# Performance work log

Measured on AMD Instinct MI355X. Metric: run time of the kernel, lower is better.

Reference implementation:

```python
import jax, jax.numpy as jnp
import numpy as np

N_ENT = 100000   # entities / graph nodes
N_REL = 500      # relations (table has 2*N_REL rows: fwd+inv)
H = 256          # hidden dim
E = 320000       # edges


def setup_inputs() -> dict:
    key = jax.random.key(0)
    ks = jax.random.split(key, 9)
    std = (2.0 / (H + H)) ** 0.5  # xavier_normal for (H,H)
    return {
        "ent_emb": jax.random.normal(ks[0], (N_ENT, H), dtype=jnp.float32),
        "rel_emb": jax.random.normal(ks[1], (2 * N_REL, H), dtype=jnp.float32),
        "w_edge": jax.random.normal(ks[2], (H, H), dtype=jnp.float32) * std,
        "w_node": jax.random.normal(ks[3], (H, H), dtype=jnp.float32) * std,
        "w_comp": jax.random.normal(ks[4], (H, H), dtype=jnp.float32) * std,
        "rel_w": jax.random.normal(ks[5], (H, H), dtype=jnp.float32) * std,
        "src": jax.random.randint(ks[6], (E,), 0, N_ENT, dtype=jnp.int32),
        "dst": jax.random.randint(ks[7], (E,), 0, N_ENT, dtype=jnp.int32),
        "rel_id": jax.random.randint(ks[8], (E,), 0, 2 * N_REL, dtype=jnp.int32),
        "node_id": jnp.arange(N_ENT, dtype=jnp.int32),
    }


def _edge_softmax(score, dst, n):
    # per-destination-node softmax over incoming edges (DGL edge_softmax)
    m = jax.ops.segment_max(score, dst, num_segments=n)
    ex = jnp.exp(score - m[dst])
    s = jax.ops.segment_sum(ex, dst, num_segments=n)
    return ex / s[dst]


def reference(ent_emb, rel_emb, w_edge, w_node, w_comp, rel_w,
              src, dst, rel_id, node_id):
    n = ent_emb.shape[0]
    h = ent_emb[node_id]          # [N, H] (node_id maps node -> entity row)
    hs = h[src]                   # [E, H] source node features
    hd = h[dst]                   # [E, H] destination node features
    e = rel_emb[rel_id]           # [E, H] edge (relation) features

    # EdgeLayer: e . h_dst -> edge_softmax -> scatter-sum(e * a) -> W -> tanh
    a_e = _edge_softmax(jnp.sum(e * hd, axis=-1), dst, n)
    edge_out = jnp.tanh(
        jax.ops.segment_sum(e * a_e[:, None], dst, num_segments=n) @ w_edge)

    # NodeLayer: h_src . h_dst -> edge_softmax -> scatter-sum(h_src * a)
    a_n = _edge_softmax(jnp.sum(hs * hd, axis=-1), dst, n)
    node_out = jnp.tanh(
        jax.ops.segment_sum(hs * a_n[:, None], dst, num_segments=n) @ w_node)

    # CompLayer (mul): comp = h_src * e ; comp . h_dst -> softmax -> scatter-sum
    comp = hs * e
    a_c = _edge_softmax(jnp.sum(comp * hd, axis=-1), dst, n)
    comp_out = jnp.tanh(
        jax.ops.segment_sum(comp * a_c[:, None], dst, num_segments=n) @ w_comp)

    out_ent = ent_emb + edge_out + node_out + comp_out
    out_rel = rel_emb @ rel_w
    return (out_ent, out_rel)
```

## Files before the change

### kernel.cpp

```cpp
#include <hip/hip_runtime.h>
#include <hip/hip_bf16.h>

#define N_ENT  100000
#define N_REL2 1000
#define H      256
#define E_EDGES 320000
#define REL_ROWS_PAD 1024
#define DEG_BINS 64

typedef unsigned short u16;
typedef short bf16x8 __attribute__((ext_vector_type(8)));
typedef float floatx4 __attribute__((ext_vector_type(4)));

__device__ __forceinline__ u16 f2bf(float f) {
    unsigned x = __float_as_uint(f);
    unsigned r = (x + 0x7fffu + ((x >> 16) & 1u)) >> 16;
    return (u16)r;
}

__device__ __forceinline__ ushort4 pack4(float4 v, float s) {
    return make_ushort4(f2bf(v.x * s), f2bf(v.y * s), f2bf(v.z * s), f2bf(v.w * s));
}

__device__ __forceinline__ float fast_tanh(float x) {
    float e = __expf(2.0f * x);
    return 1.0f - 2.0f * __builtin_amdgcn_rcpf(e + 1.0f);
}

__device__ __forceinline__ void async16(u16* lds, const u16* g) {
    __builtin_amdgcn_global_load_lds(
        (const __attribute__((address_space(1))) void*)g,
        (__attribute__((address_space(3))) void*)lds, 16, 0, 0);
}


__global__ void hist_kernel(const int* __restrict__ dst, int* __restrict__ counts) {
    int i = blockIdx.x * blockDim.x + threadIdx.x;
    if (i < E_EDGES) atomicAdd(&counts[dst[i]], 1);
}

__global__ void scan1_kernel(const int* __restrict__ counts, int* __restrict__ offsets,
                             int* __restrict__ bsum) {
    __shared__ int buf[1024];
    int t = threadIdx.x, i = blockIdx.x * 1024 + t;
    int v = (i < N_ENT) ? counts[i] : 0;
    int acc = v;
    buf[t] = acc;
    __syncthreads();
    for (int off = 1; off < 1024; off <<= 1) {
        int u = (t >= off) ? buf[t - off] : 0;
        __syncthreads();
        acc += u;
        buf[t] = acc;
        __syncthreads();
    }
    if (i < N_ENT) offsets[i] = acc - v;
    if (t == 1023) bsum[blockIdx.x] = acc;
}

__global__ void scan2_kernel(int* __restrict__ bsum, int* __restrict__ offsets) {
    __shared__ int s[128];
    int t = threadIdx.x;
    s[t] = (t < 98) ? bsum[t] : 0;
    __syncthreads();
    if (t == 0) {
        int run = 0;
        for (int b = 0; b < 98; ++b) { int x = s[b]; s[b] = run; run += x; }
        offsets[N_ENT] = run;
    }
    __syncthreads();
    if (t < 98) bsum[t] = s[t];
}

__global__ void scan3_kernel(int* __restrict__ offsets, const int* __restrict__ bsum) {
    int i = blockIdx.x * 1024 + threadIdx.x;
    if (i < N_ENT && blockIdx.x > 0) offsets[i] += bsum[blockIdx.x];
}


__global__ void deghist_kernel(const int* __restrict__ counts, int* __restrict__ dbin) {
    __shared__ int lh[DEG_BINS];
    int t = threadIdx.x;
    if (t < DEG_BINS) lh[t] = 0;
    __syncthreads();
    int i = blockIdx.x * blockDim.x + t;
    if (i < N_ENT) {
        int b = counts[i]; if (b > DEG_BINS - 1) b = DEG_BINS - 1;
        atomicAdd(&lh[b], 1);
    }
    __syncthreads();
    if (t < DEG_BINS && lh[t]) atomicAdd(&dbin[t], lh[t]);
}

__global__ void degscan_kernel(const int* __restrict__ dbin, int* __restrict__ doff) {
    if (threadIdx.x == 0) {
        int run = 0;
        for (int b = 0; b < DEG_BINS; ++b) { doff[b] = run; run += dbin[b]; }
    }
}

__global__ void degplace_kernel(const int* __restrict__ counts, int* __restrict__ doff,
                                int* __restrict__ dorder) {
    __shared__ int lh[DEG_BINS];
    __shared__ int lbase[DEG_BINS];
    int t = threadIdx.x;
    if (t < DEG_BINS) lh[t] = 0;
    __syncthreads();
    int i = blockIdx.x * blockDim.x + t;
    int b = 0, myidx = 0;
    if (i < N_ENT) {
        b = counts[i]; if (b > DEG_BINS - 1) b = DEG_BINS - 1;
        myidx = atomicAdd(&lh[b], 1);
    }
    __syncthreads();
    if (t < DEG_BINS) lbase[t] = lh[t] ? atomicAdd(&doff[t], lh[t]) : 0;
    __syncthreads();
    if (i < N_ENT) dorder[lbase[b] + myidx] = i;
}

__global__ void place_kernel(const int* __restrict__ dst, const int* __restrict__ src,
                             const int* __restrict__ rel_id, const int* __restrict__ node_id,
                             const int* __restrict__ offsets,
                             int* __restrict__ counts, int2* __restrict__ meta) {
    int i = blockIdx.x * blockDim.x + threadIdx.x;
    if (i < E_EDGES) {
        int d = dst[i];
        int old = atomicSub(&counts[d], 1);
        meta[offsets[d] + old - 1] = make_int2(node_id[src[i]], rel_id[i]);
    }
}

__global__ void swz_kernel(const float* __restrict__ w0, const float* __restrict__ w1,
                           const float* __restrict__ w2, const float* __restrict__ w3,
                           u16* __restrict__ dstp) {
    int t = blockIdx.x * blockDim.x + threadIdx.x;
    if (t >= 4 * H * H) return;
    int mat = t >> 16;
    int r = t & 65535;
    int j = r & 7, lane = (r >> 3) & 63, kstep = (r >> 9) & 7, ntile = r >> 12;
    int k = kstep * 32 + (lane >> 4) * 8 + j;
    int n = ntile * 16 + (lane & 15);
    const float* W = (mat == 0) ? w0 : (mat == 1) ? w1 : (mat == 2) ? w2 : w3;
    dstp[t] = f2bf(W[k * H + n]);
}

__global__ void relbf_kernel(const float* __restrict__ rel, u16* __restrict__ out) {
    int t = blockIdx.x * blockDim.x + threadIdx.x;
    if (t >= REL_ROWS_PAD * H) return;
    int row = t >> 8, kk = t & 255;
    int k = kk ^ ((row & 7) << 3);
    float v = (row < N_REL2) ? rel[row * H + k] : 0.f;
    out[t] = f2bf(v);
}

__global__ __launch_bounds__(256) void scatter_kernel(
    const float* __restrict__ ent, const float* __restrict__ rel,
    const int2* __restrict__ meta, const int* __restrict__ node_id,
    const int* __restrict__ offsets, const int* __restrict__ dorder,
    u16* __restrict__ agg_e, u16* __restrict__ agg_n, u16* __restrict__ agg_c) {
    int lane = threadIdx.x & 63;
    int wv = __builtin_amdgcn_readfirstlane(threadIdx.x >> 6);
    int w = blockIdx.x * 4 + wv;
    if (w >= N_ENT) return;
    int d = dorder[w];
    int nid = node_id[d];
    int p0 = offsets[d], p1 = offsets[d + 1];
    float4 hd = ((const float4*)(ent + (size_t)nid * H))[lane];
    float me = -INFINITY, mn = -INFINITY, mc = -INFINITY;
    float le = 0.f, ln = 0.f, lc = 0.f;
    float4 ae = make_float4(0, 0, 0, 0), an = make_float4(0, 0, 0, 0), ac = make_float4(0, 0, 0, 0);

    for (int pc = p0; pc < p1; pc += 4) {
        int cnt = p1 - pc; if (cnt > 4) cnt = 4;
        int2 md[4];
#pragma unroll
        for (int j = 0; j < 4; ++j) if (j < cnt) md[j] = meta[pc + j];
        float4 ev[4], sv[4];
#pragma unroll
        for (int j = 0; j < 4; ++j) if (j < cnt) {
            ev[j] = ((const float4*)(rel + (size_t)md[j].y * H))[lane];
            sv[j] = ((const float4*)(ent + (size_t)md[j].x * H))[lane];
        }
#pragma unroll
        for (int j = 0; j < 4; ++j) if (j < cnt) {
            float4 e4 = ev[j], s4 = sv[j];
            float4 c4 = make_float4(e4.x * s4.x, e4.y * s4.y, e4.z * s4.z, e4.w * s4.w);
            float de = e4.x * hd.x + e4.y * hd.y + e4.z * hd.z + e4.w * hd.w;
            float dn = s4.x * hd.x + s4.y * hd.y + s4.z * hd.z + s4.w * hd.w;
            float dc = c4.x * hd.x + c4.y * hd.y + c4.z * hd.z + c4.w * hd.w;
#pragma unroll
            for (int o = 32; o > 0; o >>= 1) {
                de += __shfl_xor(de, o);
                dn += __shfl_xor(dn, o);
                dc += __shfl_xor(dc, o);
            }
            { float nm = fmaxf(me, de); float s = __expf(me - nm); float pr = __expf(de - nm);
              le = le * s + pr;
              ae.x = ae.x * s + pr * e4.x; ae.y = ae.y * s + pr * e4.y;
              ae.z = ae.z * s + pr * e4.z; ae.w = ae.w * s + pr * e4.w; me = nm; }
            { float nm = fmaxf(mn, dn); float s = __expf(mn - nm); float pr = __expf(dn - nm);
              ln = ln * s + pr;
              an.x = an.x * s + pr * s4.x; an.y = an.y * s + pr * s4.y;
              an.z = an.z * s + pr * s4.z; an.w = an.w * s + pr * s4.w; mn = nm; }
            { float nm = fmaxf(mc, dc); float s = __expf(mc - nm); float pr = __expf(dc - nm);
              lc = lc * s + pr;
              ac.x = ac.x * s + pr * c4.x; ac.y = ac.y * s + pr * c4.y;
              ac.z = ac.z * s + pr * c4.z; ac.w = ac.w * s + pr * c4.w; mc = nm; }
        }
    }
    float ie = (le > 0.f) ? 1.0f / le : 0.f;
    float in_ = (ln > 0.f) ? 1.0f / ln : 0.f;
    float ic = (lc > 0.f) ? 1.0f / lc : 0.f;
    size_t rowb = (size_t)d * (H * 2);
    int boff = (lane * 8) ^ ((d & 7) << 4);
    *(ushort4*)((char*)agg_e + rowb + boff) = pack4(ae, ie);
    *(ushort4*)((char*)agg_n + rowb + boff) = pack4(an, in_);
    *(ushort4*)((char*)agg_c + rowb + boff) = pack4(ac, ic);
}

__global__ __launch_bounds__(256, 2) void gemm_kernel(
    const u16* __restrict__ A0, const u16* __restrict__ A1, const u16* __restrict__ A2,
    const u16* __restrict__ W0, const u16* __restrict__ W1, const u16* __restrict__ W2,
    const float* __restrict__ base, float* __restrict__ out,
    int n_real, int n_layers, int do_tanh) {
    __shared__ u16 lA[2][16384];
    int tid = threadIdx.x;
    int lane = tid & 63;
    int wv = tid >> 6;
    int m = lane & 15;
    int quad = lane >> 4;
    int r0 = blockIdx.x * 64;
    const u16* As[3] = { A0, A1, A2 };
    const u16* Ws[3] = { W0, W1, W2 };

    float outacc[4][4][4];
#pragma unroll
    for (int rt = 0; rt < 4; ++rt)
#pragma unroll
        for (int ct = 0; ct < 4; ++ct) {
            int grow = r0 + rt * 16 + quad * 4;
            int gcol = wv * 64 + ct * 16 + m;
#pragma unroll
            for (int r = 0; r < 4; ++r) {
                float v = 0.f;
                if (base != nullptr && (grow + r) < n_real) v = base[(size_t)(grow + r) * H + gcol];
                outacc[rt][ct][r] = v;
            }
        }

    {
        const u16* gsrc = As[0] + (size_t)blockIdx.x * 64 * H;
#pragma unroll
        for (int rnd = 0; rnd < 8; ++rnd) {
            int off8 = (rnd * 256 + tid) * 8;
            async16(&lA[0][off8], gsrc + off8);
        }
    }

    int mrow = m * 512;
    int swz = (m & 7) << 4;

    for (int l = 0; l < n_layers; ++l) {
        __syncthreads();
        if (l + 1 < n_layers) {
            const u16* gsrc = As[l + 1] + (size_t)blockIdx.x * 64 * H;
            u16* dstb = lA[(l + 1) & 1];
#pragma unroll
            for (int rnd = 0; rnd < 8; ++rnd) {
                int off8 = (rnd * 256 + tid) * 8;
                async16(&dstb[off8], gsrc + off8);
            }
        }
        const char* lbc = (const char*)lA[l & 1];
        const u16* Wl = Ws[l];

        floatx4 lacc[4][4];
#pragma unroll
        for (int rt = 0; rt < 4; ++rt)
#pragma unroll
            for (int ct = 0; ct < 4; ++ct)
#pragma unroll
                for (int r = 0; r < 4; ++r) lacc[rt][ct][r] = 0.f;

#pragma unroll
        for (int ks = 0; ks < 8; ++ks) {
            bf16x8 af[4], bfr[4];
#pragma unroll
            for (int rt = 0; rt < 4; ++rt)
                af[rt] = *(const bf16x8*)(lbc + rt * 8192 + mrow + ((ks * 64 + quad * 16) ^ swz));
#pragma unroll
            for (int ct = 0; ct < 4; ++ct)
                bfr[ct] = *(const bf16x8*)(Wl + (((size_t)(wv * 4 + ct) * 8 + ks) * 64 + lane) * 8);
#pragma unroll
            for (int rt = 0; rt < 4; ++rt)
#pragma unroll
                for (int ct = 0; ct < 4; ++ct)
                    lacc[rt][ct] = __builtin_amdgcn_mfma_f32_16x16x32_bf16(
                        af[rt], bfr[ct], lacc[rt][ct], 0, 0, 0);
        }

#pragma unroll
        for (int rt = 0; rt < 4; ++rt)
#pragma unroll
            for (int ct = 0; ct < 4; ++ct)
#pragma unroll
                for (int r = 0; r < 4; ++r) {
                    float v = lacc[rt][ct][r];
                    outacc[rt][ct][r] += do_tanh ? fast_tanh(v) : v;
                }
    }

#pragma unroll
    for (int rt = 0; rt < 4; ++rt)
#pragma unroll
        for (int ct = 0; ct < 4; ++ct) {
            int grow = r0 + rt * 16 + quad * 4;
            int gcol = wv * 64 + ct * 16 + m;
#pragma unroll
            for (int r = 0; r < 4; ++r)
                if ((grow + r) < n_real) out[(size_t)(grow + r) * H + gcol] = outacc[rt][ct][r];
        }
}


extern "C" void kernel_launch(void* const* d_in, const int* in_sizes, int n_in,
                              void* d_out, int out_size, void* d_ws, size_t ws_size,
                              hipStream_t stream) {
    (void)in_sizes; (void)n_in; (void)out_size; (void)ws_size;
    const float* ent    = (const float*)d_in[0];
    const float* rel    = (const float*)d_in[1];
    const float* w_edge = (const float*)d_in[2];
    const float* w_node = (const float*)d_in[3];
    const float* w_comp = (const float*)d_in[4];
    const float* rel_w  = (const float*)d_in[5];
    const int* src      = (const int*)d_in[6];
    const int* dst      = (const int*)d_in[7];
    const int* rel_id   = (const int*)d_in[8];
    const int* node_id  = (const int*)d_in[9];

    char* wsb = (char*)d_ws;
    size_t o = 0;
    auto alloc = [&](size_t bytes) -> char* {
        char* p = wsb + o;
        o = (o + bytes + 255) & ~(size_t)255;
        return p;
    };
    int* counts  = (int*)alloc((size_t)N_ENT * 4);
    int* offsets = (int*)alloc((size_t)(N_ENT + 1) * 4);
    int* bsum    = (int*)alloc(128 * 4);
    int2* meta   = (int2*)alloc((size_t)E_EDGES * 8);
    int* dbin    = (int*)alloc(DEG_BINS * 4);
    int* doff    = (int*)alloc(DEG_BINS * 4);
    int* dorder  = (int*)alloc((size_t)N_ENT * 4);
    u16* agg_e   = (u16*)alloc((size_t)N_ENT * H * 2);
    u16* agg_n   = (u16*)alloc((size_t)N_ENT * H * 2);
    u16* agg_c   = (u16*)alloc((size_t)N_ENT * H * 2);
    u16* wswz    = (u16*)alloc((size_t)4 * H * H * 2);
    u16* relbf   = (u16*)alloc((size_t)REL_ROWS_PAD * H * 2);
    (void)alloc(65536);

    float* out_ent = (float*)d_out;
    float* out_rel = out_ent + (size_t)N_ENT * H;

    hipMemsetAsync(counts, 0, (size_t)N_ENT * 4, stream);
    hipMemsetAsync(dbin, 0, DEG_BINS * 4, stream);
    hist_kernel<<<(E_EDGES + 255) / 256, 256, 0, stream>>>(dst, counts);
    scan1_kernel<<<98, 1024, 0, stream>>>(counts, offsets, bsum);
    scan2_kernel<<<1, 128, 0, stream>>>(bsum, offsets);
    scan3_kernel<<<98, 1024, 0, stream>>>(offsets, bsum);
    deghist_kernel<<<98, 1024, 0, stream>>>(counts, dbin);
    degscan_kernel<<<1, 64, 0, stream>>>(dbin, doff);
    degplace_kernel<<<98, 1024, 0, stream>>>(counts, doff, dorder);
    place_kernel<<<(E_EDGES + 255) / 256, 256, 0, stream>>>(dst, src, rel_id, node_id,
                                                            offsets, counts, meta);
    swz_kernel<<<(4 * H * H + 255) / 256, 256, 0, stream>>>(w_edge, w_node, w_comp, rel_w, wswz);
    relbf_kernel<<<(REL_ROWS_PAD * H + 255) / 256, 256, 0, stream>>>(rel, relbf);
    scatter_kernel<<<N_ENT / 4, 256, 0, stream>>>(ent, rel, meta, node_id, offsets, dorder,
                                                  agg_e, agg_n, agg_c);
    gemm_kernel<<<(N_ENT + 63) / 64, 256, 0, stream>>>(agg_e, agg_n, agg_c,
                                                       wswz, wswz + H * H, wswz + 2 * H * H,
                                                       ent, out_ent, N_ENT, 3, 1);
    gemm_kernel<<<(N_REL2 + 63) / 64, 256, 0, stream>>>(relbf, relbf, relbf,
                                                        wswz + 3 * H * H, wswz + 3 * H * H, wswz + 3 * H * H,
                                                        nullptr, out_rel, N_REL2, 1, 0);
}
```

Before: 501.7 us.

## Process four nodes per wave in scatter and fuse degree histogram into scan

The scatter kernel now gives each destination node a 16-lane group instead of a full 64-lane wave. Each lane handles 16 features in four float4 chunks, and the dot-product reductions need only four shuffle steps. This is meant to cut shuffle overhead and idle lanes on low-degree nodes, at the cost of more registers per lane and no 4-edge batching of loads. Separately, the degree histogram is folded into scan1 and the degree-bin scan into scan2, which removes two small kernel launches.

```diff
diff --git a/kernel.cpp b/kernel.cpp
--- a/kernel.cpp
+++ b/kernel.cpp
@@ -33,6 +33,21 @@
         (__attribute__((address_space(3))) void*)lds, 16, 0, 0);
 }
 
+__device__ __forceinline__ float dot4(float4 a, float4 b) {
+    return (a.x * b.x + a.y * b.y) + (a.z * b.z + a.w * b.w);
+}
+__device__ __forceinline__ float dot4m(float4 a, float4 b, float4 h) {
+    return ((a.x * b.x) * h.x + (a.y * b.y) * h.y) + ((a.z * b.z) * h.z + (a.w * b.w) * h.w);
+}
+__device__ __forceinline__ float4 sfme(float4 a, float sc, float pr, float4 v) {
+    return make_float4(a.x * sc + pr * v.x, a.y * sc + pr * v.y,
+                       a.z * sc + pr * v.z, a.w * sc + pr * v.w);
+}
+__device__ __forceinline__ float4 sfme2(float4 a, float sc, float pr, float4 u, float4 v) {
+    return make_float4(a.x * sc + (pr * u.x) * v.x, a.y * sc + (pr * u.y) * v.y,
+                       a.z * sc + (pr * u.z) * v.z, a.w * sc + (pr * u.w) * v.w);
+}
+
 
 __global__ void hist_kernel(const int* __restrict__ dst, int* __restrict__ counts) {
     int i = blockIdx.x * blockDim.x + threadIdx.x;
@@ -40,13 +55,19 @@
 }
 
 __global__ void scan1_kernel(const int* __restrict__ counts, int* __restrict__ offsets,
-                             int* __restrict__ bsum) {
+                             int* __restrict__ bsum, int* __restrict__ dbin) {
     __shared__ int buf[1024];
+    __shared__ int lh[DEG_BINS];
     int t = threadIdx.x, i = blockIdx.x * 1024 + t;
+    if (t < DEG_BINS) lh[t] = 0;
     int v = (i < N_ENT) ? counts[i] : 0;
     int acc = v;
     buf[t] = acc;
     __syncthreads();
+    if (i < N_ENT) {
+        int b = v > DEG_BINS - 1 ? DEG_BINS - 1 : v;
+        atomicAdd(&lh[b], 1);
+    }
     for (int off = 1; off < 1024; off <<= 1) {
         int u = (t >= off) ? buf[t - off] : 0;
         __syncthreads();
@@ -56,9 +77,11 @@
     }
     if (i < N_ENT) offsets[i] = acc - v;
     if (t == 1023) bsum[blockIdx.x] = acc;
-}
-
-__global__ void scan2_kernel(int* __restrict__ bsum, int* __restrict__ offsets) {
+    if (t < DEG_BINS && lh[t]) atomicAdd(&dbin[t], lh[t]);
+}
+
+__global__ void scan2_kernel(int* __restrict__ bsum, int* __restrict__ offsets,
+                             const int* __restrict__ dbin, int* __restrict__ doff) {
     __shared__ int s[128];
     int t = threadIdx.x;
     s[t] = (t < 98) ? bsum[t] : 0;
@@ -67,6 +90,8 @@
         int run = 0;
         for (int b = 0; b < 98; ++b) { int x = s[b]; s[b] = run; run += x; }
         offsets[N_ENT] = run;
+        int r2 = 0;
+        for (int b = 0; b < DEG_BINS; ++b) { int x = dbin[b]; doff[b] = r2; r2 += x; }
     }
     __syncthreads();
     if (t < 98) bsum[t] = s[t];
@@ -75,28 +100,6 @@
 __global__ void scan3_kernel(int* __restrict__ offsets, const int* __restrict__ bsum) {
     int i = blockIdx.x * 1024 + threadIdx.x;
     if (i < N_ENT && blockIdx.x > 0) offsets[i] += bsum[blockIdx.x];
-}
-
-
-__global__ void deghist_kernel(const int* __restrict__ counts, int* __restrict__ dbin) {
-    __shared__ int lh[DEG_BINS];
-    int t = threadIdx.x;
-    if (t < DEG_BINS) lh[t] = 0;
-    __syncthreads();
-    int i = blockIdx.x * blockDim.x + t;
-    if (i < N_ENT) {
-        int b = counts[i]; if (b > DEG_BINS - 1) b = DEG_BINS - 1;
-        atomicAdd(&lh[b], 1);
-    }
-    __syncthreads();
-    if (t < DEG_BINS && lh[t]) atomicAdd(&dbin[t], lh[t]);
-}
-
-__global__ void degscan_kernel(const int* __restrict__ dbin, int* __restrict__ doff) {
-    if (threadIdx.x == 0) {
-        int run = 0;
-        for (int b = 0; b < DEG_BINS; ++b) { doff[b] = run; run += dbin[b]; }
-    }
 }
 
 __global__ void degplace_kernel(const int* __restrict__ counts, int* __restrict__ doff,
@@ -159,63 +162,67 @@
     const int* __restrict__ offsets, const int* __restrict__ dorder,
     u16* __restrict__ agg_e, u16* __restrict__ agg_n, u16* __restrict__ agg_c) {
     int lane = threadIdx.x & 63;
-    int wv = __builtin_amdgcn_readfirstlane(threadIdx.x >> 6);
-    int w = blockIdx.x * 4 + wv;
-    if (w >= N_ENT) return;
+    int wv = threadIdx.x >> 6;
+    int grp = lane >> 4, sl = lane & 15;
+    int w = blockIdx.x * 16 + wv * 4 + grp;
     int d = dorder[w];
     int nid = node_id[d];
     int p0 = offsets[d], p1 = offsets[d + 1];
-    float4 hd = ((const float4*)(ent + (size_t)nid * H))[lane];
+    const float4* hrow = (const float4*)(ent + (size_t)nid * H);
+    float4 h0 = hrow[sl], h1 = hrow[16 + sl], h2 = hrow[32 + sl], h3 = hrow[48 + sl];
     float me = -INFINITY, mn = -INFINITY, mc = -INFINITY;
     float le = 0.f, ln = 0.f, lc = 0.f;
-    float4 ae = make_float4(0, 0, 0, 0), an = make_float4(0, 0, 0, 0), ac = make_float4(0, 0, 0, 0);
-
-    for (int pc = p0; pc < p1; pc += 4) {
-        int cnt = p1 - pc; if (cnt > 4) cnt = 4;
-        int2 md[4];
-#pragma unroll
-        for (int j = 0; j < 4; ++j) if (j < cnt) md[j] = meta[pc + j];
-        float4 ev[4], sv[4];
-#pragma unroll
-        for (int j = 0; j < 4; ++j) if (j < cnt) {
-            ev[j] = ((const float4*)(rel + (size_t)md[j].y * H))[lane];
-            sv[j] = ((const float4*)(ent + (size_t)md[j].x * H))[lane];
-        }
-#pragma unroll
-        for (int j = 0; j < 4; ++j) if (j < cnt) {
-            float4 e4 = ev[j], s4 = sv[j];
-            float4 c4 = make_float4(e4.x * s4.x, e4.y * s4.y, e4.z * s4.z, e4.w * s4.w);
-            float de = e4.x * hd.x + e4.y * hd.y + e4.z * hd.z + e4.w * hd.w;
-            float dn = s4.x * hd.x + s4.y * hd.y + s4.z * hd.z + s4.w * hd.w;
-            float dc = c4.x * hd.x + c4.y * hd.y + c4.z * hd.z + c4.w * hd.w;
-#pragma unroll
-            for (int o = 32; o > 0; o >>= 1) {
-                de += __shfl_xor(de, o);
-                dn += __shfl_xor(dn, o);
-                dc += __shfl_xor(dc, o);
-            }
-            { float nm = fmaxf(me, de); float s = __expf(me - nm); float pr = __expf(de - nm);
-              le = le * s + pr;
-              ae.x = ae.x * s + pr * e4.x; ae.y = ae.y * s + pr * e4.y;
-              ae.z = ae.z * s + pr * e4.z; ae.w = ae.w * s + pr * e4.w; me = nm; }
-            { float nm = fmaxf(mn, dn); float s = __expf(mn - nm); float pr = __expf(dn - nm);
-              ln = ln * s + pr;
-              an.x = an.x * s + pr * s4.x; an.y = an.y * s + pr * s4.y;
-              an.z = an.z * s + pr * s4.z; an.w = an.w * s + pr * s4.w; mn = nm; }
-            { float nm = fmaxf(mc, dc); float s = __expf(mc - nm); float pr = __expf(dc - nm);
-              lc = lc * s + pr;
-              ac.x = ac.x * s + pr * c4.x; ac.y = ac.y * s + pr * c4.y;
-              ac.z = ac.z * s + pr * c4.z; ac.w = ac.w * s + pr * c4.w; mc = nm; }
-        }
-    }
-    float ie = (le > 0.f) ? 1.0f / le : 0.f;
+    float4 z = make_float4(0.f, 0.f, 0.f, 0.f);
+    float4 ae0 = z, ae1 = z, ae2 = z, ae3 = z;
+    float4 an0 = z, an1 = z, an2 = z, an3 = z;
+    float4 ac0 = z, ac1 = z, ac2 = z, ac3 = z;
+
+    for (int pc = p0; pc < p1; ++pc) {
+        int2 md = meta[pc];
+        const float4* er = (const float4*)(rel + (size_t)md.y * H);
+        const float4* sr = (const float4*)(ent + (size_t)md.x * H);
+        float4 e0 = er[sl], e1 = er[16 + sl], e2 = er[32 + sl], e3 = er[48 + sl];
+        float4 s0 = sr[sl], s1 = sr[16 + sl], s2 = sr[32 + sl], s3 = sr[48 + sl];
+        float de = dot4(e0, h0) + dot4(e1, h1) + dot4(e2, h2) + dot4(e3, h3);
+        float dn = dot4(s0, h0) + dot4(s1, h1) + dot4(s2, h2) + dot4(s3, h3);
+        float dc = dot4m(e0, s0, h0) + dot4m(e1, s1, h1) + dot4m(e2, s2, h2) + dot4m(e3, s3, h3);
+#pragma unroll
+        for (int o = 8; o; o >>= 1) {
+            de += __shfl_xor(de, o);
+            dn += __shfl_xor(dn, o);
+            dc += __shfl_xor(dc, o);
+        }
+        { float nm = fmaxf(me, de); float sc = __expf(me - nm); float pr = __expf(de - nm);
+          le = le * sc + pr;
+          ae0 = sfme(ae0, sc, pr, e0); ae1 = sfme(ae1, sc, pr, e1);
+          ae2 = sfme(ae2, sc, pr, e2); ae3 = sfme(ae3, sc, pr, e3); me = nm; }
+        { float nm = fmaxf(mn, dn); float sc = __expf(mn - nm); float pr = __expf(dn - nm);
+          ln = ln * sc + pr;
+          an0 = sfme(an0, sc, pr, s0); an1 = sfme(an1, sc, pr, s1);
+          an2 = sfme(an2, sc, pr, s2); an3 = sfme(an3, sc, pr, s3); mn = nm; }
+        { float nm = fmaxf(mc, dc); float sc = __expf(mc - nm); float pr = __expf(dc - nm);
+          lc = lc * sc + pr;
+          ac0 = sfme2(ac0, sc, pr, e0, s0); ac1 = sfme2(ac1, sc, pr, e1, s1);
+          ac2 = sfme2(ac2, sc, pr, e2, s2); ac3 = sfme2(ac3, sc, pr, e3, s3); mc = nm; }
+    }
+    float ie  = (le > 0.f) ? 1.0f / le : 0.f;
     float in_ = (ln > 0.f) ? 1.0f / ln : 0.f;
-    float ic = (lc > 0.f) ? 1.0f / lc : 0.f;
-    size_t rowb = (size_t)d * (H * 2);
-    int boff = (lane * 8) ^ ((d & 7) << 4);
-    *(ushort4*)((char*)agg_e + rowb + boff) = pack4(ae, ie);
-    *(ushort4*)((char*)agg_n + rowb + boff) = pack4(an, in_);
-    *(ushort4*)((char*)agg_c + rowb + boff) = pack4(ac, ic);
+    float ic  = (lc > 0.f) ? 1.0f / lc : 0.f;
+    size_t rowb = (size_t)d * 512;
+    int swz = (d & 7) << 4;
+    int b0 = sl * 8;
+    *(ushort4*)((char*)agg_e + rowb + ((b0      ) ^ swz)) = pack4(ae0, ie);
+    *(ushort4*)((char*)agg_e + rowb + ((b0 + 128) ^ swz)) = pack4(ae1, ie);
+    *(ushort4*)((char*)agg_e + rowb + ((b0 + 256) ^ swz)) = pack4(ae2, ie);
+    *(ushort4*)((char*)agg_e + rowb + ((b0 + 384) ^ swz)) = pack4(ae3, ie);
+    *(ushort4*)((char*)agg_n + rowb + ((b0      ) ^ swz)) = pack4(an0, in_);
+    *(ushort4*)((char*)agg_n + rowb + ((b0 + 128) ^ swz)) = pack4(an1, in_);
+    *(ushort4*)((char*)agg_n + rowb + ((b0 + 256) ^ swz)) = pack4(an2, in_);
+    *(ushort4*)((char*)agg_n + rowb + ((b0 + 384) ^ swz)) = pack4(an3, in_);
+    *(ushort4*)((char*)agg_c + rowb + ((b0      ) ^ swz)) = pack4(ac0, ic);
+    *(ushort4*)((char*)agg_c + rowb + ((b0 + 128) ^ swz)) = pack4(ac1, ic);
+    *(ushort4*)((char*)agg_c + rowb + ((b0 + 256) ^ swz)) = pack4(ac2, ic);
+    *(ushort4*)((char*)agg_c + rowb + ((b0 + 384) ^ swz)) = pack4(ac3, ic);
 }
 
 __global__ __launch_bounds__(256, 2) void gemm_kernel(
@@ -365,18 +372,16 @@
     hipMemsetAsync(counts, 0, (size_t)N_ENT * 4, stream);
     hipMemsetAsync(dbin, 0, DEG_BINS * 4, stream);
     hist_kernel<<<(E_EDGES + 255) / 256, 256, 0, stream>>>(dst, counts);
-    scan1_kernel<<<98, 1024, 0, stream>>>(counts, offsets, bsum);
-    scan2_kernel<<<1, 128, 0, stream>>>(bsum, offsets);
+    scan1_kernel<<<98, 1024, 0, stream>>>(counts, offsets, bsum, dbin);
+    scan2_kernel<<<1, 128, 0, stream>>>(bsum, offsets, dbin, doff);
     scan3_kernel<<<98, 1024, 0, stream>>>(offsets, bsum);
-    deghist_kernel<<<98, 1024, 0, stream>>>(counts, dbin);
-    degscan_kernel<<<1, 64, 0, stream>>>(dbin, doff);
     degplace_kernel<<<98, 1024, 0, stream>>>(counts, doff, dorder);
     place_kernel<<<(E_EDGES + 255) / 256, 256, 0, stream>>>(dst, src, rel_id, node_id,
                                                             offsets, counts, meta);
     swz_kernel<<<(4 * H * H + 255) / 256, 256, 0, stream>>>(w_edge, w_node, w_comp, rel_w, wswz);
     relbf_kernel<<<(REL_ROWS_PAD * H + 255) / 256, 256, 0, stream>>>(rel, relbf);
-    scatter_kernel<<<N_ENT / 4, 256, 0, stream>>>(ent, rel, meta, node_id, offsets, dorder,
-                                                  agg_e, agg_n, agg_c);
+    scatter_kernel<<<N_ENT / 16, 256, 0, stream>>>(ent, rel, meta, node_id, offsets, dorder,
+                                                   agg_e, agg_n, agg_c);
     gemm_kernel<<<(N_ENT + 63) / 64, 256, 0, stream>>>(agg_e, agg_n, agg_c,
                                                        wswz, wswz + H * H, wswz + 2 * H * H,
                                                        ent, out_ent, N_ENT, 3, 1);
```

After: 474.1 us. 1.06x faster.
